# Kernel optimization log

Hardware: AMD Instinct MI355X
Metric: run time of the kernel (lower is better)

Reference implementation:

```python
import jax, jax.numpy as jnp
import numpy as np
from jax import lax

D3 = 48      # manifold_dim * 3
M = 512      # mem_slots
H = 256      # slot_dim
K = 32       # topk
IN = 1024    # input_dim
ODE_HID = 128
ODE_STEPS = 2
ODE_DT = 0.5
TEMP = 1.0   # temperature buffer
LN_EPS = 1e-5


def _ln(x, g, b):
    m = jnp.mean(x, axis=-1, keepdims=True)
    v = jnp.mean(jnp.square(x - m), axis=-1, keepdims=True)
    return (x - m) * lax.rsqrt(v + LN_EPS) * g + b


def setup_inputs() -> dict:
    key = jax.random.key(0)
    ks = jax.random.split(key, 12)
    s_in = 1.0 / np.sqrt(IN)
    s_h = 1.0 / np.sqrt(H)
    s_d3 = 1.0 / np.sqrt(D3)
    s_ode = 1.0 / np.sqrt(ODE_HID)
    return {
        "x": jax.random.normal(ks[0], (16, 2048, IN), jnp.float32),
        "w1": jax.random.uniform(ks[1], (IN, D3), jnp.float32, -s_in, s_in),
        "b1": jnp.zeros((D3,), jnp.float32),
        "g1": jnp.ones((D3,), jnp.float32),
        "be1": jnp.zeros((D3,), jnp.float32),
        "wa": jax.random.uniform(ks[2], (D3, ODE_HID), jnp.float32, -s_d3, s_d3),
        "ba": jnp.zeros((ODE_HID,), jnp.float32),
        "wb": jax.random.uniform(ks[3], (ODE_HID, D3), jnp.float32, -s_ode, s_ode),
        "bb": jnp.zeros((D3,), jnp.float32),
        "mem": jax.random.normal(ks[4], (M, H), jnp.float32),
        "pos": jax.random.normal(ks[5], (M, 16, 3), jnp.float32),
        "curv": jax.random.normal(ks[6], (M, 16), jnp.float32),
        "alpha": jnp.float32(0.1),
        "wo": jax.random.uniform(ks[7], (H, IN), jnp.float32, -s_h, s_h),
        "bo": jnp.zeros((IN,), jnp.float32),
        "go": jnp.ones((IN,), jnp.float32),
        "beo": jnp.zeros((IN,), jnp.float32),
    }


def reference(x, w1, b1, g1, be1, wa, ba, wb, bb, mem, pos, curv, alpha, wo, bo, go, beo):
    # manifold projection: Linear -> LayerNorm -> GELU, viewed as (B,S,D,3)
    h = jax.nn.gelu(_ln(x @ w1 + b1, g1, be1), approximate=False)  # (B,S,48)
    # ODE evolution (2 fixed steps over the flattened manifold coords)
    for _ in range(ODE_STEPS):
        dx = jnp.tanh(h @ wa + ba) @ wb + bb
        h = h + ODE_DT * dx
    # attend: query side is detached in the original
    q = lax.stop_gradient(h)                       # (B,S,48)
    mem_pos = pos.reshape(M, -1)                   # (512,48)
    # squared pairwise L2: ||q||^2 - 2 q.m + ||m||^2
    dist = (jnp.sum(q * q, axis=-1, keepdims=True)
            - 2.0 * jnp.einsum('bsd,md->bsm', q, mem_pos)
            + jnp.sum(mem_pos * mem_pos, axis=-1))
    dist = jnp.maximum(dist, 0.0) / max(TEMP, 1e-6)
    curv_w = jnp.exp(-alpha * jnp.linalg.norm(curv, axis=-1))  # (512,)
    dist = dist * curv_w[None, None, :]
    # topk smallest distances
    neg_top, itop = lax.top_k(-dist, K)            # (B,S,K)
    w = jax.nn.softmax(neg_top, axis=-1)           # softmax(-dtop)
    slots = mem[itop]                              # (B,S,K,256) gather
    attended = jnp.einsum('bsk,bskh->bsh', w, slots)
    # output projection: Linear -> LayerNorm -> GELU
    return jax.nn.gelu(_ln(attended @ wo + bo, go, beo), approximate=False)
```

## Files before the change

kernel.cpp:

```cpp
#include <hip/hip_runtime.h>
#include <stdint.h>

typedef unsigned short u16;
typedef __attribute__((ext_vector_type(4))) short short4v;
typedef __attribute__((ext_vector_type(8))) short short8v;
typedef __attribute__((ext_vector_type(4))) float f32x4;
typedef __attribute__((address_space(1))) void gv;
typedef __attribute__((address_space(3))) void lv;

#define NTOK 32768

__device__ __forceinline__ float bf2f(u16 u){ return __uint_as_float(((uint32_t)u)<<16); }
__device__ __forceinline__ u16 f2bf(float f){
  uint32_t u = __float_as_uint(f);
  u += 0x7FFFu + ((u>>16)&1u);
  return (u16)(u>>16);
}
__device__ __forceinline__ void hilo(float v, u16& h, u16& l){
  h = f2bf(v);
  l = f2bf(v - bf2f(h));
}
__device__ __forceinline__ void tsplit(float v, u16& h, u16& l){
  uint32_t b = __float_as_uint(v);
  h = (u16)(b >> 16);
  float lf = v - __uint_as_float(b & 0xFFFF0000u);
  l = (u16)(__float_as_uint(lf) >> 16);
}
__device__ __forceinline__ void tpack8(float4 a, float4 b, short8v& hi, short8v& lo){
  float v[8] = {a.x,a.y,a.z,a.w,b.x,b.y,b.z,b.w};
  #pragma unroll
  for (int i=0;i<8;++i){ u16 h,l; tsplit(v[i],h,l); hi[i]=(short)h; lo[i]=(short)l; }
}
__device__ __forceinline__ float fexp2(float x){ float r; asm("v_exp_f32 %0, %1" : "=v"(r) : "v"(x)); return r; }
__device__ __forceinline__ float frcp(float x){ float r; asm("v_rcp_f32 %0, %1" : "=v"(r) : "v"(x)); return r; }

__device__ __forceinline__ float gelu_f(float v){ return 0.5f*v*(1.0f + erff(v*0.70710678118654752440f)); }
__device__ __forceinline__ float gelu_t(float x){
  float p = x*(2.3022141f + 0.1029435f*x*x);
  float e = fexp2(p);
  float r = frcp(e + 1.0f);
  return x*(1.0f - r);
}
__device__ __forceinline__ float tanh_f(float x){
  float e = fexp2(2.8853901f*x);
  float r = frcp(e + 1.0f);
  return 1.0f - 2.0f*r;
}

__global__ __launch_bounds__(256) void k_prep(
    const float* __restrict__ w1, const float* __restrict__ wa, const float* __restrict__ wb,
    const float* __restrict__ pos, const float* __restrict__ curv,
    const float* __restrict__ mem, const float* __restrict__ wo,
    const float* __restrict__ alpha,
    u16* __restrict__ w1s, u16* __restrict__ wah, u16* __restrict__ wbh,
    float2* __restrict__ mnw,
    u16* __restrict__ memb, u16* __restrict__ woB, u16* __restrict__ posB)
{
  int i = blockIdx.x*256 + threadIdx.x;
  if (i < 49152){ int n = i>>10, k = i&1023; u16 h,l; hilo(w1[k*48+n], h, l);
                  w1s[i] = h; w1s[49152+i] = l; return; }
  i -= 49152;
  if (i < 8192){ int u = i>>6, d = i&63; float v = (d<48) ? wa[d*128+u] : 0.f;
                 u16 h,l; hilo(v,h,l); wah[i] = h; wah[8192+i] = l; return; }
  i -= 8192;
  if (i < 6144){ int n = i>>7, u = i&127; u16 h,l; hilo(wb[u*48+n], h, l);
                 wbh[i] = h; wbh[6144+i] = l; return; }
  i -= 6144;
  if (i < 512){
    float s = 0.f;
    #pragma unroll
    for (int d=0; d<48; ++d){ float v = pos[i*48+d]; s += v*v; }
    float c2 = 0.f;
    #pragma unroll
    for (int d=0; d<16; ++d){ float v = curv[i*16+d]; c2 += v*v; }
    mnw[i] = make_float2(s, expf(-alpha[0]*sqrtf(c2)));
    return;
  }
  i -= 512;
  if (i < 131072){ memb[i] = f2bf(mem[i]); return; }
  i -= 131072;
  if (i < 262144){
    int e = i & 7, ln = (i>>3)&63, n = (i>>9)&15, cpq = (i>>13)&3, kt = i>>15;
    int col = cpq*256 + n*16 + (ln & 15);
    int k   = kt*32 + (ln >> 4)*8 + e;
    woB[i] = f2bf(wo[k*1024 + col]);
    return;
  }
  i -= 262144;
  if (i < 32768){
    int e = i & 7, ln = (i>>3)&63, n = (i>>9)&31, ks = i>>14;
    int slot = n*16 + (ln&15);
    int d = ks*32 + (ln>>4)*8 + e;
    float v = (d < 48) ? pos[slot*48 + d] : 0.f;
    u16 h,l; hilo(v,h,l);
    posB[i] = h; posB[32768+i] = l;
  }
}

__global__ __launch_bounds__(256, 2) void k_proj_ode(
    const float* __restrict__ x, const u16* __restrict__ w1s,
    const float* __restrict__ b1, const float* __restrict__ g1, const float* __restrict__ be1,
    const u16* __restrict__ wah, const u16* __restrict__ wbh,
    const float* __restrict__ ba, const float* __restrict__ bb,
    float* __restrict__ hout, float* __restrict__ q2b)
{
  extern __shared__ char dynp[];
  float* xsl = (float*)dynp;
  u16* t_hi = (u16*)dynp;
  u16* t_lo = (u16*)(dynp + 16384);
  u16* h_hi = (u16*)(dynp + 32768);
  u16* h_lo = (u16*)(dynp + 40960);

  const int tid = threadIdx.x;
  const int lane = tid & 63, w = tid >> 6;
  const int l15 = lane & 15, l4 = lane >> 4;
  const int bm = blockIdx.x;
  const int arow = w*16 + l15;
  const int kb = bm & 15;

  f32x4 acc[3];
  #pragma unroll
  for (int n=0; n<3; ++n) acc[n] = (f32x4){0.f,0.f,0.f,0.f};

  auto stage_x = [&](float* dst, int kt){
    #pragma unroll
    for (int j=0; j<4; ++j){
      int idx = (j*4 + w)*64 + lane;
      int row = idx >> 4, q = idx & 15;
      int chunk = q >> 1, half = q & 1;
      const float* src = x + (size_t)(bm*64 + row)*1024 + kt*64 + ((chunk ^ (row & 7))*8 + half*4);
      __builtin_amdgcn_global_load_lds((gv*)src, (lv*)(dst + (j*4 + w)*256), 16, 0, 0);
    }
  };
  auto loadB = [&](int ktabs, short8v* Bh, short8v* Bl){
    #pragma unroll
    for (int kq=0; kq<2; ++kq)
      #pragma unroll
      for (int n=0; n<3; ++n){
        const u16* bp = w1s + (size_t)(n*16 + l15)*1024 + ktabs*64 + kq*32 + l4*8;
        Bh[kq*3+n] = *(const short8v*)bp;
        Bl[kq*3+n] = *(const short8v*)(bp + 49152);
      }
  };
  auto mfma_from = [&](const float* xb, const short8v* Bh, const short8v* Bl){
    #pragma unroll
    for (int kq=0; kq<2; ++kq){
      int chunk = kq*4 + l4;
      int phys = chunk ^ (arow & 7);
      const float* xa = xb + arow*64 + phys*8;
      float4 a0 = *(const float4*)xa;
      float4 a1 = *(const float4*)(xa + 4);
      short8v ah, al; tpack8(a0, a1, ah, al);
      #pragma unroll
      for (int n=0; n<3; ++n){
        acc[n] = __builtin_amdgcn_mfma_f32_16x16x32_bf16(ah, Bh[kq*3+n], acc[n], 0, 0, 0);
        acc[n] = __builtin_amdgcn_mfma_f32_16x16x32_bf16(ah, Bl[kq*3+n], acc[n], 0, 0, 0);
        acc[n] = __builtin_amdgcn_mfma_f32_16x16x32_bf16(al, Bh[kq*3+n], acc[n], 0, 0, 0);
      }
    }
  };

  short8v Bh0[6], Bl0[6], Bh1[6], Bl1[6];

  stage_x(xsl,         kb);
  stage_x(xsl + 4096,  (kb + 1) & 15);
  stage_x(xsl + 8192,  (kb + 2) & 15);
  loadB(kb, Bh0, Bl0);

  #pragma unroll
  for (int kt = 0; kt < 16; ++kt){
    if      (kt == 0)  asm volatile("s_waitcnt vmcnt(20)" ::: "memory");
    else if (kt == 1)  asm volatile("s_waitcnt vmcnt(32)" ::: "memory");
    else if (kt == 2)  asm volatile("s_waitcnt vmcnt(44)" ::: "memory");
    else if (kt <= 13) asm volatile("s_waitcnt vmcnt(32)" ::: "memory");
    else if (kt == 14) asm volatile("s_waitcnt vmcnt(28)" ::: "memory");
    else               asm volatile("s_waitcnt vmcnt(24)" ::: "memory");
    __builtin_amdgcn_s_barrier();
    __builtin_amdgcn_sched_barrier(0);
    if ((kt & 1) == 0){
      if (kt < 15) loadB((kt + 1 + kb) & 15, Bh1, Bl1);
      mfma_from(xsl + (kt & 3)*4096, Bh0, Bl0);
    } else {
      if (kt < 15) loadB((kt + 1 + kb) & 15, Bh0, Bl0);
      mfma_from(xsl + (kt & 3)*4096, Bh1, Bl1);
    }
    if (kt < 13) stage_x(xsl + ((kt + 3) & 3)*4096, (kt + 3 + kb) & 15);
  }

  float hreg[3][4];
  {
    float b1r[3], g1r[3], e1r[3];
    #pragma unroll
    for (int n=0; n<3; ++n){ int c = n*16 + l15; b1r[n] = b1[c]; g1r[n] = g1[c]; e1r[n] = be1[c]; }
    #pragma unroll
    for (int r=0; r<4; ++r){
      float a0 = acc[0][r] + b1r[0];
      float a1 = acc[1][r] + b1r[1];
      float a2 = acc[2][r] + b1r[2];
      float s1 = a0+a1+a2;
      float s2 = a0*a0 + a1*a1 + a2*a2;
      #pragma unroll
      for (int m=1; m<16; m<<=1){ s1 += __shfl_xor(s1, m); s2 += __shfl_xor(s2, m); }
      float mean = s1 * (1.f/48.f);
      float var  = s2 * (1.f/48.f) - mean*mean;
      float rs = rsqrtf(var + 1e-5f);
      hreg[0][r] = gelu_f((a0-mean)*rs*g1r[0] + e1r[0]);
      hreg[1][r] = gelu_f((a1-mean)*rs*g1r[1] + e1r[1]);
      hreg[2][r] = gelu_f((a2-mean)*rs*g1r[2] + e1r[2]);
    }
  }

  if (l4 < 2){
    int row = w*16 + l15;
    int ch = 6 + l4;
    int off = row*64 + (ch ^ (row & 7))*8;
    uint4 z = {0u,0u,0u,0u};
    *(uint4*)&h_hi[off] = z;
    *(uint4*)&h_lo[off] = z;
  }
  #pragma unroll
  for (int n=0; n<3; ++n)
    #pragma unroll
    for (int r=0; r<4; ++r){
      u16 hh, hl2; tsplit(hreg[n][r], hh, hl2);
      int row = w*16 + l4*4 + r;
      int col = n*16 + l15;
      int off = row*64 + ((col>>3) ^ (row & 7))*8 + (col & 7);
      h_hi[off] = hh; h_lo[off] = hl2;
    }

  float ba_r[8], bb_r[3];
  #pragma unroll
  for (int n=0; n<8; ++n) ba_r[n] = ba[n*16 + l15];
  #pragma unroll
  for (int n=0; n<3; ++n) bb_r[n] = bb[n*16 + l15];

  for (int s=0; s<2; ++s){
    f32x4 at[8];
    #pragma unroll
    for (int n=0; n<8; ++n) at[n] = (f32x4){0.f,0.f,0.f,0.f};
    #pragma unroll
    for (int kq=0; kq<2; ++kq){
      int ac = (kq*4 + l4) ^ (arow & 7);
      short8v ah = *(const short8v*)&h_hi[arow*64 + ac*8];
      short8v al = *(const short8v*)&h_lo[arow*64 + ac*8];
      #pragma unroll
      for (int n=0; n<8; ++n){
        const u16* bp = wah + (n*16 + l15)*64 + kq*32 + l4*8;
        short8v bh = *(const short8v*)bp;
        short8v bl = *(const short8v*)(bp + 8192);
        at[n] = __builtin_amdgcn_mfma_f32_16x16x32_bf16(ah, bh, at[n], 0, 0, 0);
        at[n] = __builtin_amdgcn_mfma_f32_16x16x32_bf16(ah, bl, at[n], 0, 0, 0);
        at[n] = __builtin_amdgcn_mfma_f32_16x16x32_bf16(al, bh, at[n], 0, 0, 0);
      }
    }
    #pragma unroll
    for (int n=0; n<8; ++n)
      #pragma unroll
      for (int r=0; r<4; ++r){
        float tv = tanh_f(at[n][r] + ba_r[n]);
        u16 th, tl; tsplit(tv, th, tl);
        int row = w*16 + l4*4 + r;
        int col = n*16 + l15;
        int c = col >> 3;
        int phys = (c & 8) | ((c & 7) ^ (row & 7));
        int off = row*128 + phys*8 + (col & 7);
        t_hi[off] = th; t_lo[off] = tl;
      }
    f32x4 ad[3];
    #pragma unroll
    for (int n=0; n<3; ++n) ad[n] = (f32x4){0.f,0.f,0.f,0.f};
    #pragma unroll
    for (int kq=0; kq<4; ++kq){
      int c = kq*4 + l4;
      int phys = (c & 8) | ((c & 7) ^ (arow & 7));
      short8v ah = *(const short8v*)&t_hi[arow*128 + phys*8];
      short8v al = *(const short8v*)&t_lo[arow*128 + phys*8];
      #pragma unroll
      for (int n=0; n<3; ++n){
        const u16* bp = wbh + (n*16 + l15)*128 + kq*32 + l4*8;
        short8v bh = *(const short8v*)bp;
        short8v bl = *(const short8v*)(bp + 6144);
        ad[n] = __builtin_amdgcn_mfma_f32_16x16x32_bf16(ah, bh, ad[n], 0, 0, 0);
        ad[n] = __builtin_amdgcn_mfma_f32_16x16x32_bf16(ah, bl, ad[n], 0, 0, 0);
        ad[n] = __builtin_amdgcn_mfma_f32_16x16x32_bf16(al, bh, ad[n], 0, 0, 0);
      }
    }
    #pragma unroll
    for (int n=0; n<3; ++n)
      #pragma unroll
      for (int r=0; r<4; ++r)
        hreg[n][r] += 0.5f*(ad[n][r] + bb_r[n]);
    if (s == 0){
      #pragma unroll
      for (int n=0; n<3; ++n)
        #pragma unroll
        for (int r=0; r<4; ++r){
          u16 hh, hl2; tsplit(hreg[n][r], hh, hl2);
          int row = w*16 + l4*4 + r;
          int col = n*16 + l15;
          int off = row*64 + ((col>>3) ^ (row & 7))*8 + (col & 7);
          h_hi[off] = hh; h_lo[off] = hl2;
        }
    }
  }
  #pragma unroll
  for (int r=0; r<4; ++r){
    size_t row = (size_t)(bm*64 + w*16 + l4*4 + r);
    #pragma unroll
    for (int n=0; n<3; ++n)
      hout[row*64 + n*16 + l15] = hreg[n][r];
    hout[row*64 + 48 + l15] = 0.f;
    float s2 = hreg[0][r]*hreg[0][r] + hreg[1][r]*hreg[1][r] + hreg[2][r]*hreg[2][r];
    #pragma unroll
    for (int msk=1; msk<16; msk<<=1) s2 += __shfl_xor(s2, msk);
    if (l15 == 0) q2b[row] = s2;
  }
}

__global__ __launch_bounds__(256, 4) void k_sel(
    const float* __restrict__ h, const float* __restrict__ q2b,
    const u16* __restrict__ posB, const float2* __restrict__ mnw,
    uint32_t* __restrict__ glist)
{
  __shared__ __align__(16) uint32_t tokKeys[2*4*528];

  const int tid = threadIdx.x;
  const int lane = tid & 63, w = tid >> 6;
  const int g = w >> 1, s = w & 1;
  const int l15 = lane & 15, l4 = lane >> 4;
  const int bm = blockIdx.x;

  const float* hrow = h + (size_t)(bm*32 + g*16 + l15)*64;
  float4 x0 = *(const float4*)(hrow + l4*8);
  float4 x1 = *(const float4*)(hrow + l4*8 + 4);
  float4 x2 = *(const float4*)(hrow + 32 + l4*8);
  float4 x3 = *(const float4*)(hrow + 32 + l4*8 + 4);
  short8v ah0, al0, ah1, al1;
  tpack8(x0, x1, ah0, al0);
  tpack8(x2, x3, ah1, al1);

  float4 q2v = *(const float4*)(q2b + bm*32 + g*16 + l4*4);
  float q2a[4] = {q2v.x, q2v.y, q2v.z, q2v.w};

  uint32_t kk[16][4];
  #pragma unroll
  for (int n=0; n<16; ++n){
    const u16* pb = posB + (size_t)(s*16 + n)*512 + lane*8;
    short8v bh0 = *(const short8v*)(pb);
    short8v bl0 = *(const short8v*)(pb + 32768);
    short8v bh1 = *(const short8v*)(pb + 16384);
    short8v bl1 = *(const short8v*)(pb + 49152);
    f32x4 acc = (f32x4){0.f,0.f,0.f,0.f};
    acc = __builtin_amdgcn_mfma_f32_16x16x32_bf16(ah0, bh0, acc, 0, 0, 0);
    acc = __builtin_amdgcn_mfma_f32_16x16x32_bf16(ah0, bl0, acc, 0, 0, 0);
    acc = __builtin_amdgcn_mfma_f32_16x16x32_bf16(al0, bh0, acc, 0, 0, 0);
    acc = __builtin_amdgcn_mfma_f32_16x16x32_bf16(ah1, bh1, acc, 0, 0, 0);
    acc = __builtin_amdgcn_mfma_f32_16x16x32_bf16(ah1, bl1, acc, 0, 0, 0);
    acc = __builtin_amdgcn_mfma_f32_16x16x32_bf16(al1, bh1, acc, 0, 0, 0);
    const int slot = s*256 + n*16 + l15;
    float2 mw = mnw[slot];
    #pragma unroll
    for (int r=0; r<4; ++r){
      float dd = fmaxf(q2a[r] + mw.x - 2.f*acc[r], 0.f) * mw.y;
      kk[n][r] = (__float_as_uint(dd) & 0xFFFFFE00u) | (uint32_t)slot;
    }
  }

  const int gbase = g*2112;
  const unsigned long long ltmask = (lane == 63) ? 0x7FFFFFFFFFFFFFFFull : ((1ull << lane) - 1ull);
  #pragma unroll
  for (int r=0; r<4; ++r){
    __syncthreads();
    #pragma unroll
    for (int n=0; n<16; ++n)
      tokKeys[gbase + l4*528 + s*256 + n*16 + l15] = kk[n][r];
    __syncthreads();
    uint32_t key8[2][8];
    #pragma unroll
    for (int j=0; j<2; ++j){
      *(uint4*)&key8[j][0] = *(const uint4*)&tokKeys[gbase + (s*2+j)*528 + lane*8];
      *(uint4*)&key8[j][4] = *(const uint4*)&tokKeys[gbase + (s*2+j)*528 + lane*8 + 4];
    }
    uint32_t p[2] = {0u,0u};
    for (int b=30; b>=0; --b){
      #pragma unroll
      for (int j=0; j<2; ++j){
        uint32_t c = p[j] | (1u<<b);
        int cnt = 0;
        #pragma unroll
        for (int i=0; i<8; ++i) cnt += (int)__popcll(__ballot(key8[j][i] < c));
        if (cnt <= 31) p[j] = c;
      }
    }
    #pragma unroll
    for (int j=0; j<2; ++j){
      size_t tok = (size_t)bm*32 + g*16 + (s*2+j)*4 + r;
      int base = 0;
      #pragma unroll
      for (int i=0; i<8; ++i){
        unsigned long long bal = __ballot(key8[j][i] <= p[j]);
        if (key8[j][i] <= p[j]){
          int idx = base + (int)__popcll(bal & ltmask);
          glist[tok*32 + idx] = key8[j][i];
        }
        base += (int)__popcll(bal);
      }
    }
  }
}

__global__ __launch_bounds__(256) void k_attend(
    const uint32_t* __restrict__ glist, const u16* __restrict__ memb,
    u16* __restrict__ att)
{
  const int lane = threadIdx.x & 63, w = threadIdx.x >> 6;
  const size_t tok = (size_t)blockIdx.x*4 + w;
  uint32_t lk[32];
  const uint4* lp = (const uint4*)(glist + tok*32);
  #pragma unroll
  for (int q=0; q<8; ++q) *(uint4*)&lk[q*4] = lp[q];
  uint32_t km = lk[0];
  #pragma unroll
  for (int i=1; i<32; ++i) km = min(km, lk[i]);
  const float dminf = __uint_as_float(km & 0xFFFFFE00u);

  float den = 0.f, a0=0.f, a1=0.f, a2=0.f, a3=0.f;
  #pragma unroll
  for (int i=0; i<32; ++i){
    float dk = __uint_as_float(lk[i] & 0xFFFFFE00u);
    int slot = (int)(lk[i] & 511u);
    float wg = __expf(dminf - dk);
    den += wg;
    uint2 mv = ((const uint2*)(memb + (size_t)slot*256))[lane];
    a0 += wg*bf2f((u16)(mv.x & 0xFFFFu));
    a1 += wg*bf2f((u16)(mv.x >> 16));
    a2 += wg*bf2f((u16)(mv.y & 0xFFFFu));
    a3 += wg*bf2f((u16)(mv.y >> 16));
  }
  float inv = frcp(den);
  uint32_t o0 = (uint32_t)f2bf(a0*inv) | ((uint32_t)f2bf(a1*inv) << 16);
  uint32_t o1 = (uint32_t)f2bf(a2*inv) | ((uint32_t)f2bf(a3*inv) << 16);
  ((uint2*)(att + tok*256))[lane] = make_uint2(o0, o1);
}

__global__ __launch_bounds__(1024, 4) void k_out(
    const u16* __restrict__ A, const u16* __restrict__ woB, const float* __restrict__ bo,
    const float* __restrict__ go, const float* __restrict__ beo, float* __restrict__ out)
{
  __shared__ u16 Asl[64*256];
  __shared__ float redS1[64][65];
  __shared__ float redS2[64][65];
  __shared__ float finM[64], finR[64];

  const int tid = threadIdx.x;
  const int lane = tid & 63, w = tid >> 6;
  const int l15 = lane & 15, l4 = lane >> 4;
  const int bm = blockIdx.x;

  #pragma unroll
  for (int j=0; j<2; ++j){
    int idx = j*1024 + tid;
    int row = idx >> 5, ch = idx & 31;
    int gc = (ch & 24) | ((ch & 7) ^ (row & 7));
    uint4 v = *(const uint4*)(A + (size_t)(bm*64 + row)*256 + gc*8);
    *(uint4*)&Asl[row*256 + ch*8] = v;
  }
  __syncthreads();

  f32x4 acc[4][4];
  #pragma unroll
  for (int m=0; m<4; ++m)
    #pragma unroll
    for (int n=0; n<4; ++n) acc[m][n] = (f32x4){0.f,0.f,0.f,0.f};

  #pragma unroll
  for (int kt=0; kt<8; ++kt){
    const int c = kt*4 + l4;
    short8v af[4];
    #pragma unroll
    for (int m=0; m<4; ++m){
      int arow = m*16 + l15;
      int aphys = (c & 24) | ((c & 7) ^ (arow & 7));
      af[m] = *(const short8v*)&Asl[arow*256 + aphys*8];
    }
    const u16* bbase = woB + ((size_t)kt*64 + w*4)*512 + lane*8;
    #pragma unroll
    for (int n=0; n<4; ++n){
      short8v bf = *(const short8v*)(bbase + n*512);
      #pragma unroll
      for (int m=0; m<4; ++m)
        acc[m][n] = __builtin_amdgcn_mfma_f32_16x16x32_bf16(af[m], bf, acc[m][n], 0, 0, 0);
    }
  }

  float bor[4];
  #pragma unroll
  for (int n=0; n<4; ++n) bor[n] = bo[w*64 + n*16 + l15];

  float s1[4][4], s2[4][4];
  #pragma unroll
  for (int m=0; m<4; ++m)
    #pragma unroll
    for (int r=0; r<4; ++r){ s1[m][r] = 0.f; s2[m][r] = 0.f; }
  #pragma unroll
  for (int m=0; m<4; ++m)
    #pragma unroll
    for (int n=0; n<4; ++n)
      #pragma unroll
      for (int r=0; r<4; ++r){
        float v = acc[m][n][r] + bor[n];
        acc[m][n][r] = v;
        s1[m][r] += v; s2[m][r] += v*v;
      }
  #pragma unroll
  for (int m=0; m<4; ++m)
    #pragma unroll
    for (int r=0; r<4; ++r){
      s1[m][r] += __shfl_xor(s1[m][r], 1);
      s2[m][r] += __shfl_xor(s2[m][r], 1);
      s1[m][r] += __shfl_xor(s1[m][r], 2);
      s2[m][r] += __shfl_xor(s2[m][r], 2);
    }
  if ((l15 & 3) == 0){
    int q = l15 >> 2;
    #pragma unroll
    for (int m=0; m<4; ++m)
      #pragma unroll
      for (int r=0; r<4; ++r){
        int row = m*16 + l4*4 + r;
        redS1[row][w*4 + q] = s1[m][r];
        redS2[row][w*4 + q] = s2[m][r];
      }
  }
  __syncthreads();

  {
    int row = w*4 + (lane >> 4);
    int p0 = lane & 15;
    float a1 = redS1[row][p0] + redS1[row][p0+16] + redS1[row][p0+32] + redS1[row][p0+48];
    float a2 = redS2[row][p0] + redS2[row][p0+16] + redS2[row][p0+32] + redS2[row][p0+48];
    #pragma unroll
    for (int msk=1; msk<16; msk<<=1){
      a1 += __shfl_xor(a1, msk);
      a2 += __shfl_xor(a2, msk);
    }
    if (p0 == 0){
      float mu = a1 * (1.f/1024.f);
      float var = a2 * (1.f/1024.f) - mu*mu;
      finM[row] = mu;
      finR[row] = rsqrtf(var + 1e-5f);
    }
  }
  __syncthreads();

  float4 muv[4], rsv[4];
  #pragma unroll
  for (int m=0; m<4; ++m){
    muv[m] = *(const float4*)&finM[m*16 + l4*4];
    rsv[m] = *(const float4*)&finR[m*16 + l4*4];
  }

  float gor[4], eor[4];
  #pragma unroll
  for (int n=0; n<4; ++n){
    int col = w*64 + n*16 + l15;
    gor[n] = go[col]; eor[n] = beo[col];
  }
  #pragma unroll
  for (int m=0; m<4; ++m)
    #pragma unroll
    for (int r=0; r<4; ++r){
      size_t row = (size_t)bm*64 + m*16 + l4*4 + r;
      float* op = out + row*1024 + w*64 + l15;
      float mu = ((const float*)&muv[m])[r];
      float rv = ((const float*)&rsv[m])[r];
      #pragma unroll
      for (int n=0; n<4; ++n){
        op[n*16] = gelu_t((acc[m][n][r] - mu)*rv*gor[n] + eor[n]);
      }
    }
}

extern "C" void kernel_launch(void* const* d_in, const int* in_sizes, int n_in,
                              void* d_out, int out_size, void* d_ws, size_t ws_size,
                              hipStream_t stream) {
  const float* x    = (const float*)d_in[0];
  const float* w1   = (const float*)d_in[1];
  const float* b1   = (const float*)d_in[2];
  const float* g1   = (const float*)d_in[3];
  const float* be1  = (const float*)d_in[4];
  const float* wa   = (const float*)d_in[5];
  const float* ba   = (const float*)d_in[6];
  const float* wb   = (const float*)d_in[7];
  const float* bb   = (const float*)d_in[8];
  const float* mem  = (const float*)d_in[9];
  const float* pos  = (const float*)d_in[10];
  const float* curv = (const float*)d_in[11];
  const float* alpha= (const float*)d_in[12];
  const float* wo   = (const float*)d_in[13];
  const float* bo   = (const float*)d_in[14];
  const float* go   = (const float*)d_in[15];
  const float* beo  = (const float*)d_in[16];
  float* out = (float*)d_out;

  char* ws = (char*)d_ws;
  size_t o = 0;
  auto take = [&](size_t b) -> char* { char* p = ws + o; o += (b + 255) & ~(size_t)255; return p; };
  char*  regA   = take(67108864);
  float* hbuf64 = (float*)(regA + 6291456);
  float* q2b    = (float*)(regA + 6291456 + 8388608);
  u16*   att    = (u16*)take(16777216);
  u16*   w1s    = (u16*)take(196608);
  u16*   wah    = (u16*)take(32768);
  u16*   wbh    = (u16*)take(24576);
  float2* mnw   = (float2*)take(4096);
  u16*   memb   = (u16*)take(262144);
  u16*   woB    = (u16*)take(524288);
  u16*   posB   = (u16*)take(131072);
  uint32_t* glist = (uint32_t*)take(4194304);

  hipFuncSetAttribute((const void*)k_proj_ode, hipFuncAttributeMaxDynamicSharedMemorySize, 65536);

  k_prep<<<1914, 256, 0, stream>>>(w1, wa, wb, pos, curv, mem, wo, alpha,
                                   w1s, wah, wbh, mnw, memb, woB, posB);
  k_proj_ode<<<512, 256, 65536, stream>>>(x, w1s, b1, g1, be1, wah, wbh, ba, bb,
                                          hbuf64, q2b);
  k_sel<<<1024, 256, 0, stream>>>(hbuf64, q2b, posB, mnw, glist);
  k_attend<<<8192, 256, 0, stream>>>(glist, memb, att);
  k_out<<<512, 1024, 0, stream>>>(att, woB, bo, go, beo, out);
  (void)in_sizes; (void)n_in; (void)out_size; (void)ws_size;
}
```

Measured before the change: 250.3 us.

## Replace 4-stage rotating x pipeline with bulk 4-tile staging per phase

Replaces the rotating 4-buffer LDS ring, which overlapped x loads with MFMA using tuned per-iteration vmcnt waits, with a simpler scheme. Each of 4 phases loads 4 K-tiles of x into LDS at once, waits for all loads, then runs 4 MFMA steps while double-buffering the w1 B fragments in registers. It also drops the per-block K rotation offset (kb). This gives up overlap between x loads and compute, and removing the rotation may make many blocks read the same w1 region at the same moment.

```diff
diff --git a/kernel.cpp b/kernel.cpp
--- a/kernel.cpp
+++ b/kernel.cpp
@@ -116,28 +116,33 @@
   const int l15 = lane & 15, l4 = lane >> 4;
   const int bm = blockIdx.x;
   const int arow = w*16 + l15;
-  const int kb = bm & 15;
 
   f32x4 acc[3];
   #pragma unroll
   for (int n=0; n<3; ++n) acc[n] = (f32x4){0.f,0.f,0.f,0.f};
 
-  auto stage_x = [&](float* dst, int kt){
-    #pragma unroll
-    for (int j=0; j<4; ++j){
-      int idx = (j*4 + w)*64 + lane;
-      int row = idx >> 4, q = idx & 15;
-      int chunk = q >> 1, half = q & 1;
-      const float* src = x + (size_t)(bm*64 + row)*1024 + kt*64 + ((chunk ^ (row & 7))*8 + half*4);
-      __builtin_amdgcn_global_load_lds((gv*)src, (lv*)(dst + (j*4 + w)*256), 16, 0, 0);
+  auto stage_x4 = [&](int s){
+    #pragma unroll
+    for (int j=0; j<16; ++j){
+      int i = j*4 + w;
+      int O = i*256 + lane*4;
+      int ktl    = O >> 12;
+      int rem    = O & 4095;
+      int row    = rem >> 6;
+      int within = rem & 63;
+      int chunk  = within >> 3;
+      int half   = (within >> 2) & 1;
+      int phys   = chunk ^ (row & 7);
+      const float* src = x + (size_t)(bm*64 + row)*1024 + s*256 + ktl*64 + phys*8 + half*4;
+      __builtin_amdgcn_global_load_lds((gv*)src, (lv*)(xsl + i*256), 16, 0, 0);
     }
   };
-  auto loadB = [&](int ktabs, short8v* Bh, short8v* Bl){
+  auto loadB = [&](int kt, short8v* Bh, short8v* Bl){
     #pragma unroll
     for (int kq=0; kq<2; ++kq)
       #pragma unroll
       for (int n=0; n<3; ++n){
-        const u16* bp = w1s + (size_t)(n*16 + l15)*1024 + ktabs*64 + kq*32 + l4*8;
+        const u16* bp = w1s + (size_t)(n*16 + l15)*1024 + kt*64 + kq*32 + l4*8;
         Bh[kq*3+n] = *(const short8v*)bp;
         Bl[kq*3+n] = *(const short8v*)(bp + 49152);
       }
@@ -160,32 +165,25 @@
     }
   };
 
-  short8v Bh0[6], Bl0[6], Bh1[6], Bl1[6];
-
-  stage_x(xsl,         kb);
-  stage_x(xsl + 4096,  (kb + 1) & 15);
-  stage_x(xsl + 8192,  (kb + 2) & 15);
-  loadB(kb, Bh0, Bl0);
-
-  #pragma unroll
-  for (int kt = 0; kt < 16; ++kt){
-    if      (kt == 0)  asm volatile("s_waitcnt vmcnt(20)" ::: "memory");
-    else if (kt == 1)  asm volatile("s_waitcnt vmcnt(32)" ::: "memory");
-    else if (kt == 2)  asm volatile("s_waitcnt vmcnt(44)" ::: "memory");
-    else if (kt <= 13) asm volatile("s_waitcnt vmcnt(32)" ::: "memory");
-    else if (kt == 14) asm volatile("s_waitcnt vmcnt(28)" ::: "memory");
-    else               asm volatile("s_waitcnt vmcnt(24)" ::: "memory");
+  short8v BhA[6], BlA[6], BhB[6], BlB[6];
+  loadB(0, BhA, BlA);
+
+  for (int s = 0; s < 4; ++s){
+    if (s) __syncthreads();
+    stage_x4(s);
+    asm volatile("s_waitcnt vmcnt(0)" ::: "memory");
     __builtin_amdgcn_s_barrier();
     __builtin_amdgcn_sched_barrier(0);
-    if ((kt & 1) == 0){
-      if (kt < 15) loadB((kt + 1 + kb) & 15, Bh1, Bl1);
-      mfma_from(xsl + (kt & 3)*4096, Bh0, Bl0);
-    } else {
-      if (kt < 15) loadB((kt + 1 + kb) & 15, Bh0, Bl0);
-      mfma_from(xsl + (kt & 3)*4096, Bh1, Bl1);
-    }
-    if (kt < 13) stage_x(xsl + ((kt + 3) & 3)*4096, (kt + 3 + kb) & 15);
-  }
+    loadB(4*s + 1, BhB, BlB);
+    mfma_from(xsl,          BhA, BlA);
+    loadB(4*s + 2, BhA, BlA);
+    mfma_from(xsl + 4096,   BhB, BlB);
+    loadB(4*s + 3, BhB, BlB);
+    mfma_from(xsl + 8192,   BhA, BlA);
+    if (s < 3) loadB(4*s + 4, BhA, BlA);
+    mfma_from(xsl + 12288,  BhB, BlB);
+  }
+  __syncthreads();
 
   float hreg[3][4];
   {
```

After: 265.3 us. 1.06x slower.
